# Kernel optimization log

Measured on AMD Instinct MI355X. Metric: run time of the kernel, lower is better.

## Reference

```python
import jax, jax.numpy as jnp
import numpy as np

N_USERS = 200000
N_MOVIES = 80000
N = N_USERS + N_MOVIES
H = 64
F_MOVIE = 20
E = 1250000
EL = 500000


def setup_inputs() -> dict:
    key = jax.random.key(0)
    ks = jax.random.split(key, 13)
    s = 0.05
    inp = {
        "movie_x": jax.random.normal(ks[0], (N_MOVIES, F_MOVIE), jnp.float32),
        "user_emb": jax.random.normal(ks[1], (N_USERS, H), jnp.float32) * s,
        "movie_emb": jax.random.normal(ks[2], (N_MOVIES, H), jnp.float32) * s,
        "lin_W": jax.random.normal(ks[3], (H, F_MOVIE), jnp.float32) * s,
        "lin_b": jax.random.normal(ks[4], (H,), jnp.float32) * s,
        "W1l": jax.random.normal(ks[5], (H, H), jnp.float32) * s,
        "b1": jax.random.normal(ks[6], (H,), jnp.float32) * s,
        "W1r": jax.random.normal(ks[7], (H, H), jnp.float32) * s,
        "W2l": jax.random.normal(ks[8], (H, H), jnp.float32) * s,
        "b2": jax.random.normal(ks[9], (H,), jnp.float32) * s,
        "W2r": jax.random.normal(ks[10], (H, H), jnp.float32) * s,
        "edge_index": jax.random.randint(ks[11], (2, E), 0, N, jnp.int64),
        "edge_label_index": jnp.stack([
            jax.random.randint(jax.random.fold_in(ks[12], 0), (EL,), 0, N_USERS, jnp.int64),
            jax.random.randint(jax.random.fold_in(ks[12], 1), (EL,), 0, N_MOVIES, jnp.int64),
        ]),
    }
    return inp


def _sage(x, src, dst, Wl, bl, Wr):
    # PyG SAGEConv, mean aggregation: lin_l(mean_{j->i} x_j) + lin_r(x_i)
    msg = x[src]  # [E, H] gather
    agg = jax.ops.segment_sum(msg, dst, num_segments=N)  # [N, H] scatter-add
    deg = jax.ops.segment_sum(jnp.ones((src.shape[0],), x.dtype), dst, num_segments=N)
    mean = agg / jnp.maximum(deg, 1.0)[:, None]
    return mean @ Wl.T + bl + x @ Wr.T


def reference(movie_x, user_emb, movie_emb, lin_W, lin_b,
              W1l, b1, W1r, W2l, b2, W2r, edge_index, edge_label_index):
    # encode: users = embedding lookup (node_id == arange), movies = linear(x) + embedding
    x_user = user_emb
    x_movie = movie_x @ lin_W.T + lin_b + movie_emb
    x = jnp.concatenate([x_user, x_movie], axis=0)  # [N, H]

    src, dst = edge_index[0], edge_index[1]
    x = jax.nn.relu(_sage(x, src, dst, W1l, b1, W1r))
    x = _sage(x, src, dst, W2l, b2, W2r)

    xu = x[:N_USERS]
    xm = x[N_USERS:]
    # dot-product edge scoring over supervision edges
    u = xu[edge_label_index[0]]  # [EL, H]
    m = xm[edge_label_index[1]]  # [EL, H]
    return jnp.sum(u * m, axis=-1)  # [EL]
```

## Files before the change

kernel.cpp:

```cpp
#include <hip/hip_runtime.h>
#include <hip/hip_bf16.h>

#define NU 200000
#define NM 80000
#define NT 280000
#define HD 64
#define FM 20

#define BSHIFT 10
#define NBUCK ((NT + 1023) >> 10)
#define CHUNK 2048
#define HCHUNK 4096

typedef __attribute__((ext_vector_type(8))) short short8;
typedef __attribute__((ext_vector_type(4))) float floatx4;

__device__ __forceinline__ float bfu2f(unsigned short u) {
    union { unsigned int u; float f; } c; c.u = ((unsigned int)u) << 16; return c.f;
}

__device__ __forceinline__ unsigned short f2bf_raw(float f) {
    union { float f; unsigned int u; } c; c.f = f;
    unsigned int u = c.u + 0x7FFFu + ((c.u >> 16) & 1u);
    return (unsigned short)(u >> 16);
}

__device__ __forceinline__ float ldf(const void* p, long i, int isbf) {
    return isbf ? bfu2f(((const unsigned short*)p)[i]) : ((const float*)p)[i];
}
__device__ __forceinline__ int ldidx(const int* p, long j, int is64) {
    return is64 ? p[2 * j] : p[j];
}

__global__ void probe_kernel(const void* user_emb, const int* ei, int* flags) {
    int t = threadIdx.x;
    int bad = 0;
    for (int i = t; i < 128; i += 64) {
        unsigned short h = ((const unsigned short*)user_emb)[i];
        unsigned int e = (h >> 7) & 0xFF;
        if (e >= 135) bad = 1;
    }
    unsigned long long mf = __ballot(bad != 0);
    int odd_nonzero = 0;
    if (t < 16 && ei[2 * t + 1] != 0) odd_nonzero = 1;
    unsigned long long mi = __ballot(odd_nonzero != 0);
    if (t == 0) {
        flags[0] = (mf == 0) ? 1 : 0;
        flags[1] = (mi == 0) ? 1 : 0;
    }
}

__global__ __launch_bounds__(256) void prep_user(
    const void* __restrict__ user_emb,
    unsigned short* __restrict__ xb,
    const int* __restrict__ flags)
{
    long t = (long)blockIdx.x * 256 + threadIdx.x;
    int isbf = flags[0];
    if (isbf) {
        ((short8*)xb)[t] = ((const short8*)user_emb)[t];
    } else {
        floatx4 a = ((const floatx4*)user_emb)[2 * t];
        floatx4 b = ((const floatx4*)user_emb)[2 * t + 1];
        short8 r;
        r[0] = (short)f2bf_raw(a[0]); r[1] = (short)f2bf_raw(a[1]);
        r[2] = (short)f2bf_raw(a[2]); r[3] = (short)f2bf_raw(a[3]);
        r[4] = (short)f2bf_raw(b[0]); r[5] = (short)f2bf_raw(b[1]);
        r[6] = (short)f2bf_raw(b[2]); r[7] = (short)f2bf_raw(b[3]);
        ((short8*)xb)[t] = r;
    }
}

__global__ __launch_bounds__(256) void prep_movie(
    const void* __restrict__ movie_x,
    const void* __restrict__ movie_emb,
    const void* __restrict__ lin_W,
    const void* __restrict__ lin_b,
    unsigned short* __restrict__ xb,
    const int* __restrict__ flags)
{
    int isbf = flags[0];
    int tid = threadIdx.x;
    int lane = tid & 63;
    int wave = blockIdx.x * 4 + (tid >> 6);
    int m0 = __builtin_amdgcn_readfirstlane(wave << 2);
    if (m0 >= NM) return;

    float wr[FM];
    if (isbf) {
        const unsigned int* p = (const unsigned int*)((const unsigned short*)lin_W + (long)lane * FM);
        #pragma unroll
        for (int i = 0; i < FM / 2; ++i) {
            unsigned int u = p[i];
            wr[2 * i]     = bfu2f((unsigned short)(u & 0xFFFFu));
            wr[2 * i + 1] = bfu2f((unsigned short)(u >> 16));
        }
    } else {
        const floatx4* p = (const floatx4*)((const float*)lin_W + (long)lane * FM);
        #pragma unroll
        for (int i = 0; i < FM / 4; ++i) {
            floatx4 v = p[i];
            wr[4 * i] = v[0]; wr[4 * i + 1] = v[1]; wr[4 * i + 2] = v[2]; wr[4 * i + 3] = v[3];
        }
    }
    float bias = ldf(lin_b, lane, isbf);

    #pragma unroll
    for (int mm = 0; mm < 4; ++mm) {
        int m = m0 + mm;
        float a0 = bias + ldf(movie_emb, (long)m * HD + lane, isbf);
        float a1 = 0.f, a2 = 0.f, a3 = 0.f;
        if (isbf) {
            const unsigned int* mr = (const unsigned int*)((const unsigned short*)movie_x + (long)m * FM);
            #pragma unroll
            for (int kk = 0; kk < FM / 2; ++kk) {
                unsigned int u = mr[kk];
                float x0 = bfu2f((unsigned short)(u & 0xFFFFu));
                float x1 = bfu2f((unsigned short)(u >> 16));
                if (kk & 1) { a2 += x0 * wr[2 * kk]; a3 += x1 * wr[2 * kk + 1]; }
                else        { a0 += x0 * wr[2 * kk]; a1 += x1 * wr[2 * kk + 1]; }
            }
        } else {
            const float* mr = (const float*)movie_x + (long)m * FM;
            #pragma unroll
            for (int k = 0; k < FM; k += 4) {
                a0 += mr[k]     * wr[k];
                a1 += mr[k + 1] * wr[k + 1];
                a2 += mr[k + 2] * wr[k + 2];
                a3 += mr[k + 3] * wr[k + 3];
            }
        }
        xb[(long)(NU + m) * HD + lane] = f2bf_raw((a0 + a1) + (a2 + a3));
    }
}

__global__ __launch_bounds__(256) void bucket_hist(
    const int* __restrict__ ei, int E,
    int* __restrict__ bcnt,
    const int* __restrict__ flags)
{
    __shared__ int h[NBUCK];
    int tid = threadIdx.x;
    for (int i = tid; i < NBUCK; i += 256) h[i] = 0;
    __syncthreads();
    int is64 = flags[1];
    long e0 = (long)blockIdx.x * HCHUNK;
    long e1 = e0 + HCHUNK; if (e1 > E) e1 = E;
    for (long j = e0 + tid; j < e1; j += 256) {
        int d = ldidx(ei, (long)E + j, is64);
        atomicAdd(&h[d >> BSHIFT], 1);
    }
    __syncthreads();
    for (int i = tid; i < NBUCK; i += 256)
        if (h[i]) atomicAdd(&bcnt[i], h[i]);
}

__global__ __launch_bounds__(256) void bucket_scan(
    const int* __restrict__ bcnt, int* __restrict__ bstart, int E)
{
    __shared__ int s[256];
    int t = threadIdx.x;
    int a0 = (2 * t     < NBUCK) ? bcnt[2 * t]     : 0;
    int a1 = (2 * t + 1 < NBUCK) ? bcnt[2 * t + 1] : 0;
    s[t] = a0 + a1;
    __syncthreads();
    for (int off = 1; off < 256; off <<= 1) {
        int v = s[t];
        if (t >= off) v += s[t - off];
        __syncthreads();
        s[t] = v;
        __syncthreads();
    }
    int run = (t == 0) ? 0 : s[t - 1];
    if (2 * t     < NBUCK) bstart[2 * t]     = run;
    if (2 * t + 1 < NBUCK) bstart[2 * t + 1] = run + a0;
    if (t == 0) bstart[NBUCK] = E;
}

__global__ __launch_bounds__(256) void bucket_kernel(
    const int* __restrict__ ei, int E,
    const int* __restrict__ bstart,
    int* __restrict__ bfill,
    int* __restrict__ packed,
    const int* __restrict__ flags)
{
    __shared__ int histw[4][NBUCK];
    __shared__ int curw[4][NBUCK];
    __shared__ int wbase[NBUCK];

    int tid = threadIdx.x;
    int w = tid >> 6;
    int lane = tid & 63;
    int is64 = flags[1];
    long e0 = (long)blockIdx.x * CHUNK;
    long rem = (long)E - e0;
    int n = (rem < CHUNK) ? (int)rem : CHUNK;
    if (n <= 0) return;

    for (int i = tid; i < NBUCK; i += 256) {
        histw[0][i] = 0; histw[1][i] = 0; histw[2][i] = 0; histw[3][i] = 0;
        curw[0][i] = 0;  curw[1][i] = 0;  curw[2][i] = 0;  curw[3][i] = 0;
    }
    __syncthreads();

    int jbeg = w * (CHUNK / 4);
    int jend = jbeg + (CHUNK / 4); if (jend > n) jend = n;
    for (int j = jbeg + lane; j < jend; j += 64) {
        int d = ldidx(ei, (long)E + e0 + j, is64);
        atomicAdd(&histw[w][d >> BSHIFT], 1);
    }
    __syncthreads();

    for (int b = tid; b < NBUCK; b += 256) {
        int h0 = histw[0][b], h1 = histw[1][b], h2 = histw[2][b], h3 = histw[3][b];
        int hb = h0 + h1 + h2 + h3;
        int g = (hb > 0) ? atomicAdd(&bfill[b], hb) : 0;
        wbase[b] = bstart[b] + g;
        histw[0][b] = 0;
        histw[1][b] = h0;
        histw[2][b] = h0 + h1;
        histw[3][b] = h0 + h1 + h2;
    }
    __syncthreads();

    for (int j = jbeg + lane; j < jend; j += 64) {
        int s = ldidx(ei, e0 + j, is64);
        int d = ldidx(ei, (long)E + e0 + j, is64);
        int b = d >> BSHIFT;
        int pos = atomicAdd(&curw[w][b], 1);
        packed[wbase[b] + histw[w][b] + pos] = (s << BSHIFT) | (d & ((1 << BSHIFT) - 1));
    }
}

__global__ __launch_bounds__(256) void finefill_kernel(
    const int* __restrict__ bstart,
    const int* __restrict__ packed,
    int* __restrict__ rowptr,
    int* __restrict__ cnt,
    int* __restrict__ srclist)
{
    __shared__ int lcnt[1 << BSHIFT];
    __shared__ int lsum[256];
    int b = blockIdx.x;
    int tid = threadIdx.x;
    int nbase = b << BSHIFT;
    int beg = bstart[b];
    int end = bstart[b + 1];

    for (int i = tid; i < (1 << BSHIFT); i += 256) lcnt[i] = 0;
    __syncthreads();

    for (int j = beg + tid; j < end; j += 256)
        atomicAdd(&lcnt[packed[j] & ((1 << BSHIFT) - 1)], 1);
    __syncthreads();

    int i0 = tid * 4;
    int c0 = lcnt[i0], c1 = lcnt[i0 + 1], c2 = lcnt[i0 + 2], c3 = lcnt[i0 + 3];
    lsum[tid] = c0 + c1 + c2 + c3;
    __syncthreads();
    for (int off = 1; off < 256; off <<= 1) {
        int v = lsum[tid];
        if (tid >= off) v += lsum[tid - off];
        __syncthreads();
        lsum[tid] = v;
        __syncthreads();
    }
    int run = beg + ((tid == 0) ? 0 : lsum[tid - 1]);
    int r0 = run, r1 = r0 + c0, r2 = r1 + c1, r3 = r2 + c2;

    int n0 = nbase + i0;
    if (n0     < NT) { rowptr[n0]     = r0; cnt[n0]     = c0; }
    if (n0 + 1 < NT) { rowptr[n0 + 1] = r1; cnt[n0 + 1] = c1; }
    if (n0 + 2 < NT) { rowptr[n0 + 2] = r2; cnt[n0 + 2] = c2; }
    if (n0 + 3 < NT) { rowptr[n0 + 3] = r3; cnt[n0 + 3] = c3; }

    lcnt[i0] = r0; lcnt[i0 + 1] = r1; lcnt[i0 + 2] = r2; lcnt[i0 + 3] = r3;
    __syncthreads();

    for (int j = beg + tid; j < end; j += 256) {
        int p = packed[j];
        int dl = p & ((1 << BSHIFT) - 1);
        int pos = atomicAdd(&lcnt[dl], 1);
        srclist[pos] = p >> BSHIFT;
    }
}

__global__ __launch_bounds__(256) void gather_mean(
    const unsigned short* __restrict__ x,
    const int* __restrict__ rowptr,
    const int* __restrict__ cnt,
    const int* __restrict__ srclist,
    unsigned short* __restrict__ meanb)
{
    int wid = (blockIdx.x * 256 + threadIdx.x) >> 6;
    int lane = threadIdx.x & 63;
    int g = lane >> 2;
    int sub = lane & 3;
    int n = wid * 16 + g;
    if (n >= NT) return;
    int beg = rowptr[n];
    int deg = cnt[n];

    float acc[16];
    #pragma unroll
    for (int k = 0; k < 16; ++k) acc[k] = 0.f;

    for (int j0 = 0; j0 < deg; j0 += 4) {
        int e = j0 + sub;
        int sv = (e < deg) ? srclist[beg + e] : 0;
        int cq = deg - j0; if (cq > 4) cq = 4;
        short8 r[4][2];
        #pragma unroll
        for (int q = 0; q < 4; ++q) {
            int s = __shfl(sv, (g << 2) | q);
            const short8* p = (const short8*)&x[(long)s * HD + sub * 16];
            r[q][0] = p[0];
            r[q][1] = p[1];
        }
        #pragma unroll
        for (int q = 0; q < 4; ++q) {
            if (q < cq) {
                #pragma unroll
                for (int k = 0; k < 8; ++k) {
                    acc[k]     += bfu2f((unsigned short)r[q][0][k]);
                    acc[k + 8] += bfu2f((unsigned short)r[q][1][k]);
                }
            }
        }
    }

    float rd = 1.0f / fmaxf((float)deg, 1.0f);
    short8 o0, o1;
    #pragma unroll
    for (int k = 0; k < 8; ++k) {
        o0[k] = (short)f2bf_raw(acc[k] * rd);
        o1[k] = (short)f2bf_raw(acc[k + 8] * rd);
    }
    short8* op = (short8*)&meanb[(long)n * HD + sub * 16];
    op[0] = o0;
    op[1] = o1;
}

template <bool RELU>
__global__ __launch_bounds__(256) void combine_kernel(
    const unsigned short* __restrict__ meanb,
    const unsigned short* __restrict__ xin,
    const void* __restrict__ Wl,
    const void* __restrict__ bias,
    const void* __restrict__ Wr,
    unsigned short* __restrict__ out,
    const int* __restrict__ flags)
{
    __shared__ short8 lWl8[HD * HD / 8];
    __shared__ short8 lWr8[HD * HD / 8];
    __shared__ short8 lmean8[HD * HD / 8];
    __shared__ short8 lx8[HD * HD / 8];
    __shared__ float lb[HD];
    unsigned short* lWl  = (unsigned short*)lWl8;
    unsigned short* lWr  = (unsigned short*)lWr8;
    unsigned short* lmean = (unsigned short*)lmean8;
    unsigned short* lx   = (unsigned short*)lx8;

    int tid = threadIdx.x;
    int isbf = flags[0];
    if (isbf) {
        const short8* wl8 = (const short8*)Wl;
        const short8* wr8 = (const short8*)Wr;
        for (int i = tid; i < HD * HD / 8; i += 256) { lWl8[i] = wl8[i]; lWr8[i] = wr8[i]; }
    } else {
        const floatx4* wlf = (const floatx4*)Wl;
        const floatx4* wrf = (const floatx4*)Wr;
        for (int i = tid; i < HD * HD / 8; i += 256) {
            floatx4 a = wlf[2 * i], b = wlf[2 * i + 1];
            short8 r;
            r[0]=(short)f2bf_raw(a[0]); r[1]=(short)f2bf_raw(a[1]); r[2]=(short)f2bf_raw(a[2]); r[3]=(short)f2bf_raw(a[3]);
            r[4]=(short)f2bf_raw(b[0]); r[5]=(short)f2bf_raw(b[1]); r[6]=(short)f2bf_raw(b[2]); r[7]=(short)f2bf_raw(b[3]);
            lWl8[i] = r;
            a = wrf[2 * i]; b = wrf[2 * i + 1];
            r[0]=(short)f2bf_raw(a[0]); r[1]=(short)f2bf_raw(a[1]); r[2]=(short)f2bf_raw(a[2]); r[3]=(short)f2bf_raw(a[3]);
            r[4]=(short)f2bf_raw(b[0]); r[5]=(short)f2bf_raw(b[1]); r[6]=(short)f2bf_raw(b[2]); r[7]=(short)f2bf_raw(b[3]);
            lWr8[i] = r;
        }
    }
    if (tid < HD) lb[tid] = ldf(bias, tid, isbf);

    int tile = blockIdx.x;
    long base = (long)tile * HD * HD;
    const short8* mv = (const short8*)(meanb + base);
    const short8* xv = (const short8*)(xin + base);
    for (int i = tid; i < HD * HD / 8; i += 256) { lmean8[i] = mv[i]; lx8[i] = xv[i]; }
    __syncthreads();

    int w = tid >> 6;
    int lane = tid & 63;
    int mrow = lane & 15;
    int quad = lane >> 4;

    short8 am0 = *(const short8*)&lmean[(w * 16 + mrow) * HD + quad * 8];
    short8 am1 = *(const short8*)&lmean[(w * 16 + mrow) * HD + 32 + quad * 8];
    short8 ax0 = *(const short8*)&lx[(w * 16 + mrow) * HD + quad * 8];
    short8 ax1 = *(const short8*)&lx[(w * 16 + mrow) * HD + 32 + quad * 8];

    floatx4 acc[4];
    #pragma unroll
    for (int ht = 0; ht < 4; ++ht) {
        int h = ht * 16 + mrow;
        short8 bl0 = *(const short8*)&lWl[h * HD + quad * 8];
        short8 bl1 = *(const short8*)&lWl[h * HD + 32 + quad * 8];
        short8 br0 = *(const short8*)&lWr[h * HD + quad * 8];
        short8 br1 = *(const short8*)&lWr[h * HD + 32 + quad * 8];
        floatx4 a = {0.f, 0.f, 0.f, 0.f};
        a = __builtin_amdgcn_mfma_f32_16x16x32_bf16(am0, bl0, a, 0, 0, 0);
        a = __builtin_amdgcn_mfma_f32_16x16x32_bf16(am1, bl1, a, 0, 0, 0);
        a = __builtin_amdgcn_mfma_f32_16x16x32_bf16(ax0, br0, a, 0, 0, 0);
        a = __builtin_amdgcn_mfma_f32_16x16x32_bf16(ax1, br1, a, 0, 0, 0);
        acc[ht] = a;
    }

    #pragma unroll
    for (int ht = 0; ht < 4; ++ht) {
        int h = ht * 16 + mrow;
        float bv = lb[h];
        #pragma unroll
        for (int r = 0; r < 4; ++r) {
            int node = w * 16 + quad * 4 + r;
            float v = acc[ht][r] + bv;
            if (RELU) v = fmaxf(v, 0.0f);
            out[base + node * HD + h] = f2bf_raw(v);
        }
    }
}

__global__ __launch_bounds__(256) void dot_kernel(
    const unsigned short* __restrict__ x2,
    const int* __restrict__ eli,
    void* __restrict__ out,
    int EL,
    const int* __restrict__ flags)
{
    int wid = (blockIdx.x * 256 + threadIdx.x) >> 6;
    long base = (long)wid * 16;
    if (base >= EL) return;
    int lane = threadIdx.x & 63;
    int isbf = flags[0];
    int is64 = flags[1];

    int idxv = 0;
    if (lane < 16)      idxv = ldidx(eli, base + lane, is64);
    else if (lane < 32) idxv = ldidx(eli, (long)EL + base + (lane - 16), is64);

    int e   = lane >> 2;
    int seg = lane & 3;
    int u = __shfl(idxv, e);
    int m = __shfl(idxv, 16 + e);

    const short8* up = (const short8*)(x2 + (long)u * HD + seg * 16);
    const short8* mp = (const short8*)(x2 + (long)(NU + m) * HD + seg * 16);
    short8 a0 = up[0], a1 = up[1];
    short8 b0 = mp[0], b1 = mp[1];

    float p = 0.f;
    #pragma unroll
    for (int j = 0; j < 8; ++j) {
        p += bfu2f((unsigned short)a0[j]) * bfu2f((unsigned short)b0[j]);
        p += bfu2f((unsigned short)a1[j]) * bfu2f((unsigned short)b1[j]);
    }
    p += __shfl_xor(p, 1);
    p += __shfl_xor(p, 2);

    if (seg == 0) {
        long g = base + e;
        if (isbf) ((unsigned short*)out)[g] = f2bf_raw(p);
        else      ((float*)out)[g] = p;
    }
}

extern "C" void kernel_launch(void* const* d_in, const int* in_sizes, int n_in,
                              void* d_out, int out_size, void* d_ws, size_t ws_size,
                              hipStream_t stream)
{
    const void* movie_x   = d_in[0];
    const void* user_emb  = d_in[1];
    const void* movie_emb = d_in[2];
    const void* lin_W     = d_in[3];
    const void* lin_b     = d_in[4];
    const void* W1l       = d_in[5];
    const void* b1        = d_in[6];
    const void* W1r       = d_in[7];
    const void* W2l       = d_in[8];
    const void* b2        = d_in[9];
    const void* W2r       = d_in[10];
    const int* ei  = (const int*)d_in[11];
    const int* eli = (const int*)d_in[12];
    int E  = in_sizes[11] / 2;
    int EL = in_sizes[12] / 2;

    char* w = (char*)d_ws;
    unsigned short* xb      = (unsigned short*)w;  w += (size_t)NT * HD * 2;
    unsigned short* meanb   = (unsigned short*)w;  w += (size_t)NT * HD * 2;
    int*            cnt     = (int*)w;             w += (size_t)NT * 4;
    int*            rowptr  = (int*)w;             w += (size_t)NT * 4;
    int*            srclist = (int*)w;             w += (size_t)E * 4;
    int*            packed  = (int*)w;             w += (size_t)E * 4;
    int*            bcnt    = (int*)w;             w += (size_t)(NBUCK + 1) * 4;
    int*            bstart  = (int*)w;             w += (size_t)(NBUCK + 1) * 4;
    int*            bfill   = (int*)w;             w += (size_t)NBUCK * 4;
    int*            flags   = (int*)w;

    const int user_blocks   = (NU * HD / 8) / 256;
    const int movie_blocks  = NM / 16;
    const int hist_blocks   = (E + HCHUNK - 1) / HCHUNK;
    const int bucket_blocks = (E + CHUNK - 1) / CHUNK;
    const int gather_blocks = ((NT / 16) * 64 + 255) / 256;
    const int tile_blocks   = NT / 64;
    const int dot_blocks    = ((EL + 15) / 16 + 3) / 4;

    probe_kernel<<<1, 64, 0, stream>>>(user_emb, ei, flags);

    prep_user<<<user_blocks, 256, 0, stream>>>(user_emb, xb, flags);
    prep_movie<<<movie_blocks, 256, 0, stream>>>(movie_x, movie_emb, lin_W, lin_b, xb, flags);

    hipMemsetAsync(bcnt, 0, (size_t)(NBUCK + 1) * 4, stream);
    hipMemsetAsync(bfill, 0, (size_t)NBUCK * 4, stream);
    bucket_hist<<<hist_blocks, 256, 0, stream>>>(ei, E, bcnt, flags);
    bucket_scan<<<1, 256, 0, stream>>>(bcnt, bstart, E);
    bucket_kernel<<<bucket_blocks, 256, 0, stream>>>(ei, E, bstart, bfill, packed, flags);
    finefill_kernel<<<NBUCK, 256, 0, stream>>>(bstart, packed, rowptr, cnt, srclist);

    gather_mean<<<gather_blocks, 256, 0, stream>>>(xb, rowptr, cnt, srclist, meanb);
    combine_kernel<true><<<tile_blocks, 256, 0, stream>>>(meanb, xb, W1l, b1, W1r, xb, flags);

    gather_mean<<<gather_blocks, 256, 0, stream>>>(xb, rowptr, cnt, srclist, meanb);
    combine_kernel<false><<<tile_blocks, 256, 0, stream>>>(meanb, xb, W2l, b2, W2r, xb, flags);

    dot_kernel<<<dot_blocks, 256, 0, stream>>>(xb, eli, d_out, EL, flags);
}
```

Before: 356.1 us.

## Replace atomic bucket fill with per-block histograms and column prefix scan

Edge bucketing now writes a per-block bucket histogram, scans each bucket's column across blocks to get deterministic per-block offsets, and scatters edges using those offsets. This drops the global atomic bfill reservation, the per-wave local histogram pass inside the scatter kernel, and the two memsets. In exchange it adds an extra col_scan kernel launch and a NSB×NBUCK workspace array. Within-block ordering still comes from shared atomics.

```diff
diff --git a/kernel.cpp b/kernel.cpp
--- a/kernel.cpp
+++ b/kernel.cpp
@@ -9,8 +9,7 @@
 
 #define BSHIFT 10
 #define NBUCK ((NT + 1023) >> 10)
-#define CHUNK 2048
-#define HCHUNK 4096
+#define SCHUNK 4096
 
 typedef __attribute__((ext_vector_type(8))) short short8;
 typedef __attribute__((ext_vector_type(4))) float floatx4;
@@ -134,25 +133,58 @@
     }
 }
 
-__global__ __launch_bounds__(256) void bucket_hist(
+__global__ __launch_bounds__(512) void blk_hist(
     const int* __restrict__ ei, int E,
-    int* __restrict__ bcnt,
+    int* __restrict__ blkhist,
     const int* __restrict__ flags)
 {
     __shared__ int h[NBUCK];
     int tid = threadIdx.x;
-    for (int i = tid; i < NBUCK; i += 256) h[i] = 0;
+    for (int i = tid; i < NBUCK; i += 512) h[i] = 0;
     __syncthreads();
     int is64 = flags[1];
-    long e0 = (long)blockIdx.x * HCHUNK;
-    long e1 = e0 + HCHUNK; if (e1 > E) e1 = E;
-    for (long j = e0 + tid; j < e1; j += 256) {
+    long e0 = (long)blockIdx.x * SCHUNK;
+    long e1 = e0 + SCHUNK; if (e1 > E) e1 = E;
+    for (long j = e0 + tid; j < e1; j += 512) {
         int d = ldidx(ei, (long)E + j, is64);
         atomicAdd(&h[d >> BSHIFT], 1);
     }
     __syncthreads();
-    for (int i = tid; i < NBUCK; i += 256)
-        if (h[i]) atomicAdd(&bcnt[i], h[i]);
+    long obase = (long)blockIdx.x * NBUCK;
+    for (int i = tid; i < NBUCK; i += 512) blkhist[obase + i] = h[i];
+}
+
+__global__ __launch_bounds__(256) void col_scan(
+    int* __restrict__ blkhist, int NSB,
+    int* __restrict__ bcnt)
+{
+    __shared__ int larr[2048];
+    __shared__ int lsum[256];
+    int b = blockIdx.x;
+    int t = threadIdx.x;
+    for (int i = t; i < NSB; i += 256) larr[i] = blkhist[(long)i * NBUCK + b];
+    __syncthreads();
+    int C = (NSB + 255) >> 8;
+    int beg = t * C;
+    int end = beg + C; if (end > NSB) end = NSB; if (beg > NSB) beg = NSB;
+    int s = 0;
+    for (int i = beg; i < end; ++i) s += larr[i];
+    lsum[t] = s;
+    __syncthreads();
+    for (int off = 1; off < 256; off <<= 1) {
+        int v = lsum[t];
+        if (t >= off) v += lsum[t - off];
+        __syncthreads();
+        lsum[t] = v;
+        __syncthreads();
+    }
+    int run = (t == 0) ? 0 : lsum[t - 1];
+    for (int i = beg; i < end; ++i) {
+        int v = larr[i];
+        blkhist[(long)i * NBUCK + b] = run;
+        run += v;
+    }
+    if (t == 0) bcnt[b] = lsum[255];
 }
 
 __global__ __launch_bounds__(256) void bucket_scan(
@@ -177,58 +209,27 @@
     if (t == 0) bstart[NBUCK] = E;
 }
 
-__global__ __launch_bounds__(256) void bucket_kernel(
+__global__ __launch_bounds__(512) void scatter_kernel(
     const int* __restrict__ ei, int E,
     const int* __restrict__ bstart,
-    int* __restrict__ bfill,
+    const int* __restrict__ blkhist,
     int* __restrict__ packed,
     const int* __restrict__ flags)
 {
-    __shared__ int histw[4][NBUCK];
-    __shared__ int curw[4][NBUCK];
-    __shared__ int wbase[NBUCK];
-
+    __shared__ int cur[NBUCK];
     int tid = threadIdx.x;
-    int w = tid >> 6;
-    int lane = tid & 63;
+    long obase = (long)blockIdx.x * NBUCK;
+    for (int i = tid; i < NBUCK; i += 512) cur[i] = bstart[i] + blkhist[obase + i];
+    __syncthreads();
     int is64 = flags[1];
-    long e0 = (long)blockIdx.x * CHUNK;
-    long rem = (long)E - e0;
-    int n = (rem < CHUNK) ? (int)rem : CHUNK;
-    if (n <= 0) return;
-
-    for (int i = tid; i < NBUCK; i += 256) {
-        histw[0][i] = 0; histw[1][i] = 0; histw[2][i] = 0; histw[3][i] = 0;
-        curw[0][i] = 0;  curw[1][i] = 0;  curw[2][i] = 0;  curw[3][i] = 0;
-    }
-    __syncthreads();
-
-    int jbeg = w * (CHUNK / 4);
-    int jend = jbeg + (CHUNK / 4); if (jend > n) jend = n;
-    for (int j = jbeg + lane; j < jend; j += 64) {
-        int d = ldidx(ei, (long)E + e0 + j, is64);
-        atomicAdd(&histw[w][d >> BSHIFT], 1);
-    }
-    __syncthreads();
-
-    for (int b = tid; b < NBUCK; b += 256) {
-        int h0 = histw[0][b], h1 = histw[1][b], h2 = histw[2][b], h3 = histw[3][b];
-        int hb = h0 + h1 + h2 + h3;
-        int g = (hb > 0) ? atomicAdd(&bfill[b], hb) : 0;
-        wbase[b] = bstart[b] + g;
-        histw[0][b] = 0;
-        histw[1][b] = h0;
-        histw[2][b] = h0 + h1;
-        histw[3][b] = h0 + h1 + h2;
-    }
-    __syncthreads();
-
-    for (int j = jbeg + lane; j < jend; j += 64) {
-        int s = ldidx(ei, e0 + j, is64);
-        int d = ldidx(ei, (long)E + e0 + j, is64);
+    long e0 = (long)blockIdx.x * SCHUNK;
+    long e1 = e0 + SCHUNK; if (e1 > E) e1 = E;
+    for (long j = e0 + tid; j < e1; j += 512) {
+        int s = ldidx(ei, j, is64);
+        int d = ldidx(ei, (long)E + j, is64);
         int b = d >> BSHIFT;
-        int pos = atomicAdd(&curw[w][b], 1);
-        packed[wbase[b] + histw[w][b] + pos] = (s << BSHIFT) | (d & ((1 << BSHIFT) - 1));
+        int pos = atomicAdd(&cur[b], 1);
+        packed[pos] = (s << BSHIFT) | (d & ((1 << BSHIFT) - 1));
     }
 }
 
@@ -495,6 +496,8 @@
     int E  = in_sizes[11] / 2;
     int EL = in_sizes[12] / 2;
 
+    const int NSB = (E + SCHUNK - 1) / SCHUNK;
+
     char* w = (char*)d_ws;
     unsigned short* xb      = (unsigned short*)w;  w += (size_t)NT * HD * 2;
     unsigned short* meanb   = (unsigned short*)w;  w += (size_t)NT * HD * 2;
@@ -504,13 +507,11 @@
     int*            packed  = (int*)w;             w += (size_t)E * 4;
     int*            bcnt    = (int*)w;             w += (size_t)(NBUCK + 1) * 4;
     int*            bstart  = (int*)w;             w += (size_t)(NBUCK + 1) * 4;
-    int*            bfill   = (int*)w;             w += (size_t)NBUCK * 4;
+    int*            blkhist = (int*)w;             w += (size_t)NSB * NBUCK * 4;
     int*            flags   = (int*)w;
 
     const int user_blocks   = (NU * HD / 8) / 256;
     const int movie_blocks  = NM / 16;
-    const int hist_blocks   = (E + HCHUNK - 1) / HCHUNK;
-    const int bucket_blocks = (E + CHUNK - 1) / CHUNK;
     const int gather_blocks = ((NT / 16) * 64 + 255) / 256;
     const int tile_blocks   = NT / 64;
     const int dot_blocks    = ((EL + 15) / 16 + 3) / 4;
@@ -520,11 +521,10 @@
     prep_user<<<user_blocks, 256, 0, stream>>>(user_emb, xb, flags);
     prep_movie<<<movie_blocks, 256, 0, stream>>>(movie_x, movie_emb, lin_W, lin_b, xb, flags);
 
-    hipMemsetAsync(bcnt, 0, (size_t)(NBUCK + 1) * 4, stream);
-    hipMemsetAsync(bfill, 0, (size_t)NBUCK * 4, stream);
-    bucket_hist<<<hist_blocks, 256, 0, stream>>>(ei, E, bcnt, flags);
+    blk_hist<<<NSB, 512, 0, stream>>>(ei, E, blkhist, flags);
+    col_scan<<<NBUCK, 256, 0, stream>>>(blkhist, NSB, bcnt);
     bucket_scan<<<1, 256, 0, stream>>>(bcnt, bstart, E);
-    bucket_kernel<<<bucket_blocks, 256, 0, stream>>>(ei, E, bstart, bfill, packed, flags);
+    scatter_kernel<<<NSB, 512, 0, stream>>>(ei, E, bstart, blkhist, packed, flags);
     finefill_kernel<<<NBUCK, 256, 0, stream>>>(bstart, packed, rowptr, cnt, srclist);
 
     gather_mean<<<gather_blocks, 256, 0, stream>>>(xb, rowptr, cnt, srclist, meanb);
```

After: 327.2 us. 1.09x faster.
